# Kernel tuning notes

Measured on AMD Instinct MI355X. Metric: run time of the kernel, lower is better.

Reference implementation:

```python
import math
import jax
import jax.numpy as jnp
import numpy as np

LMAX = 6                 # lmax
F8, F2 = 16, 64          # f_out//8, f_out//2 for f_out=128
DIM6 = sum((2 * l + 1) ** 2 for l in range(LMAX + 1))  # 455 = dim of so3_irreps(6)
NA = NB = NG = 16        # SO(3) activation grid (alpha, beta, gamma)
B, T, H, C = 32, 16, 4, 128


def _real_sh(lmax, xyz):
    # real spherical harmonics: (N,3) unit vectors -> (N,(lmax+1)^2), m=-l..l per l
    x, y, z = xyz[:, 0], xyz[:, 1], xyz[:, 2]
    st = np.sqrt(np.clip(1.0 - z * z, 0.0, None))
    phi = np.arctan2(y, x)
    n = xyz.shape[0]
    P = np.zeros((lmax + 1, lmax + 1, n))
    P[0, 0] = 1.0
    for m in range(1, lmax + 1):
        P[m, m] = -(2 * m - 1) * st * P[m - 1, m - 1]
    for m in range(lmax):
        P[m + 1, m] = (2 * m + 1) * z * P[m, m]
    for m in range(lmax + 1):
        for l in range(m + 2, lmax + 1):
            P[l, m] = ((2 * l - 1) * z * P[l - 1, m] - (l + m - 1) * P[l - 2, m]) / (l - m)
    cols = []
    for l in range(lmax + 1):
        for m in range(-l, l + 1):
            am = abs(m)
            K = math.sqrt((2 * l + 1) / (4 * math.pi) * math.factorial(l - am) / math.factorial(l + am))
            if m > 0:
                cols.append(math.sqrt(2.0) * K * np.cos(m * phi) * P[l, m])
            elif m < 0:
                cols.append(math.sqrt(2.0) * K * np.sin(am * phi) * P[l, am])
            else:
                cols.append(K * P[l, 0])
    return np.stack(cols, axis=-1)


def _flat_wigner(lmax, Rs):
    # component-normalized flat real Wigner-D basis: (G,3,3) -> (G, sum_l (2l+1)^2)
    # D_l(R) solved from Y_l(R x) = D_l(R) Y_l(x) by least squares in float64
    rng = np.random.default_rng(0)
    pts = rng.normal(size=(32, 3))
    pts /= np.linalg.norm(pts, axis=1, keepdims=True)
    Y = _real_sh(lmax, pts)                                     # (32,(lmax+1)^2)
    rp = np.einsum('gij,nj->gni', Rs, pts).reshape(-1, 3)
    Yr = _real_sh(lmax, rp).reshape(len(Rs), 32, -1)            # (G,32,(lmax+1)^2)
    blocks = []
    for l in range(lmax + 1):
        d = 2 * l + 1
        o = l * l
        Apinv = np.linalg.pinv(Y[:, o:o + d])                   # (d,32)
        D = np.einsum('kn,gnm->gmk', Apinv, Yr[:, :, o:o + d])  # (G,d,d)
        blocks.append(math.sqrt(d) * D.reshape(len(Rs), d * d))
    return np.concatenate(blocks, axis=-1)


def _rz(a):
    c, s = np.cos(a), np.sin(a)
    z, o = np.zeros_like(a), np.ones_like(a)
    return np.stack([np.stack([c, -s, z], -1), np.stack([s, c, z], -1), np.stack([z, z, o], -1)], -2)


def _ry(a):
    c, s = np.cos(a), np.sin(a)
    z, o = np.zeros_like(a), np.ones_like(a)
    return np.stack([np.stack([c, z, s], -1), np.stack([z, o, z], -1), np.stack([-s, z, c], -1)], -2)


def _so3_grid():
    # ZYZ Euler grid, Gauss-Legendre in beta; rotations (G,3,3) + Haar weights (G,) summing to 1
    nodes, wts = np.polynomial.legendre.leggauss(NB)
    betas = np.arccos(nodes)
    alphas = np.arange(NA) * 2 * np.pi / NA
    gammas = np.arange(NG) * 2 * np.pi / NG
    Aa, Bb, Cg = np.meshgrid(alphas, betas, gammas, indexing='ij')
    Rs = _rz(Aa.ravel()) @ _ry(Bb.ravel()) @ _rz(Cg.ravel())
    w = np.broadcast_to(wts[None, :, None], (NA, NB, NG)).ravel().copy()
    w *= (2 * np.pi / NA) * (2 * np.pi / NG) / (8 * np.pi ** 2)
    return Rs, w


def _ico_rotations():
    # the 60 rotations of the icosahedral group, generated by closure
    phi = (1.0 + 5.0 ** 0.5) / 2.0
    def rot(axis, ang):
        a = np.asarray(axis, dtype=np.float64)
        a = a / np.linalg.norm(a)
        K = np.array([[0.0, -a[2], a[1]], [a[2], 0.0, -a[0]], [-a[1], a[0], 0.0]])
        return np.eye(3) + math.sin(ang) * K + (1.0 - math.cos(ang)) * (K @ K)
    gens = [rot([0.0, 1.0, phi], 2.0 * np.pi / 5.0), rot([0.0, 0.0, 1.0], np.pi)]
    elems = [np.eye(3)]
    seen = {tuple(np.round(np.eye(3), 5).ravel())}
    frontier = list(elems)
    while frontier:
        nxt = []
        for R in frontier:
            for g in gens:
                Q = g @ R
                k = tuple(np.round(Q, 5).ravel())
                if k not in seen:
                    seen.add(k)
                    elems.append(Q)
                    nxt.append(Q)
        frontier = nxt
    return np.stack(elems)


def _equi_linear(xl, wl):
    # e3nn-style per-irrep linear: xl (...,f_in,u,m), wl (f_in,f_out,u,v); fan_in = f_in*u
    fan_in = wl.shape[0] * wl.shape[2]
    return jnp.einsum('...fum,fguv->...gvm', xl, wl) / np.sqrt(fan_in)


def _forward(x, trajectory, w1s, w1v, w2, D_in, D_outw, ico_wigners):
    b, t, _ = trajectory.shape
    # pack '1x0e+3x1e': scalar = traj[...,9], vectors = traj[...,:9]
    s = trajectory[..., 9][..., None, None, None]       # (b,t,f=1,u=1,m=1)
    v = trajectory[..., :9].reshape(b, t, 1, 3, 3)      # (b,t,f=1,u=3,m=3)
    h = jnp.concatenate([_equi_linear(s, w1s).reshape(b, t, F8, 1),
                         _equi_linear(v, w1v).reshape(b, t, F8, 9)], axis=-1)  # (b,t,16,10)
    # SO(3) activation: coeffs -> grid signal -> relu -> coeffs (lmax 1 -> 6)
    sig = jax.nn.relu(jnp.einsum('btci,gi->btcg', h, D_in))
    h = jnp.einsum('btcg,gi->btci', sig, D_outw)        # (b,t,16,455)
    # per-l equivariant linear, f 16 -> 64
    outs = []
    o = 0
    for l in range(LMAX + 1):
        d = 2 * l + 1
        xl = h[..., o:o + d * d].reshape(b, t, F8, d, d)
        outs.append(_equi_linear(xl, w2[l]).reshape(b, t, F2, d * d))
        o += d * d
    traj = jnp.concatenate(outs, axis=-1)               # (b,t,64,455)
    traj = jnp.einsum('bhcj,ij->bhci', traj, ico_wigners)  # sample on ico rotations
    xg = jnp.einsum('bhcj,ij->bhci', x, ico_wigners)
    return xg, traj


def setup_inputs():
    key = jax.random.key(0)
    ks = jax.random.split(key, 11)
    Rs, w = _so3_grid()
    D_in = _flat_wigner(1, Rs).astype(np.float32)                      # (G,10)
    D_outw = (_flat_wigner(LMAX, Rs) * w[:, None]).astype(np.float32)  # (G,455)
    ico = _flat_wigner(LMAX, _ico_rotations()).astype(np.float32)      # (60,455)
    inp = dict(
        x=jax.random.normal(ks[0], (B, H, C, DIM6), jnp.float32),
        trajectory=jax.random.normal(ks[1], (B, T, 10), jnp.float32),
        w1s=jax.random.normal(ks[2], (1, F8, 1, 1), jnp.float32),
        w1v=jax.random.normal(ks[3], (1, F8, 3, 3), jnp.float32),
        D_in=jnp.asarray(D_in),
        D_outw=jnp.asarray(D_outw),
        ico_wigners=jnp.asarray(ico),
    )
    for l in range(LMAX + 1):
        inp['w2_%d' % l] = jax.random.normal(ks[4 + l], (F8, F2, 2 * l + 1, 2 * l + 1), jnp.float32)
    return inp


def reference(x, trajectory, w1s, w1v, w2_0, w2_1, w2_2, w2_3, w2_4, w2_5, w2_6, D_in, D_outw, ico_wigners):
    w2 = [w2_0, w2_1, w2_2, w2_3, w2_4, w2_5, w2_6]
    return _forward(x, trajectory, w1s, w1v, w2, D_in, D_outw, ico_wigners)
```

## Files before the change

kernel.cpp:

```cpp
#include <hip/hip_runtime.h>
#include <math.h>


#define NBT  512
#define F8c  16
#define F2c  64
#define GJ   455
#define GG   4096
#define NICO 60
#define JP   512

typedef short bf16x8 __attribute__((ext_vector_type(8)));
typedef float f32x4  __attribute__((ext_vector_type(4)));
typedef unsigned int u32;
typedef unsigned short ushort;

struct W7 { const float* p[7]; };

__device__ __forceinline__ ushort f2bf(float f) {
  u32 u = __float_as_uint(f);
  return (ushort)((u + 0x7fffu + ((u >> 16) & 1u)) >> 16);
}

__device__ __forceinline__ int sel7(int l, int a0, int a1, int a2, int a3,
                                    int a4, int a5, int a6) {
  int r = a6;
  r = (l == 5) ? a5 : r; r = (l == 4) ? a4 : r; r = (l == 3) ? a3 : r;
  r = (l == 2) ? a2 : r; r = (l == 1) ? a1 : r; r = (l == 0) ? a0 : r;
  return r;
}

__global__ __launch_bounds__(256) void k_hic(const float* __restrict__ traj,
                                             const float* __restrict__ w1s,
                                             const float* __restrict__ w1v,
                                             const float* __restrict__ ico,
                                             float* __restrict__ h,
                                             ushort* __restrict__ icoB) {
  if (blockIdx.x < 320) {
    int idx = blockIdx.x * 256 + threadIdx.x;
    if (idx >= NBT * 160) return;
    int bt = idx / 160, r = idx % 160, c = r / 10, i = r % 10;
    const float* tr = traj + bt * 10;
    float val;
    if (i == 0) {
      val = tr[9] * w1s[c];
    } else {
      int k = i - 1, v = k / 3, m = k % 3;
      float s = 0.f;
      #pragma unroll
      for (int u = 0; u < 3; ++u) s = fmaf(tr[u * 3 + m], w1v[c * 9 + u * 3 + v], s);
      val = s * 0.57735026918962576f;
    }
    h[idx] = val;
  } else {
    int e = (blockIdx.x - 320) * 256 + threadIdx.x;
    int i = e >> 9, j = e & 511;
    icoB[e] = (i < NICO && j < GJ) ? f2bf(ico[i * GJ + j]) : (ushort)0;
  }
}

__global__ __launch_bounds__(256) void k_bt(const float* __restrict__ Dout,
                                            ushort* __restrict__ DoutBT) {
  __shared__ float t[64][65];
  int jt = blockIdx.x, kt = blockIdx.y;
  int tx = threadIdx.x & 63, ty = threadIdx.x >> 6;
  #pragma unroll
  for (int i = 0; i < 16; ++i) {
    int r = i * 4 + ty, j = jt * 64 + tx;
    t[r][tx] = (j < GJ) ? Dout[(size_t)(kt * 64 + r) * GJ + j] : 0.f;
  }
  __syncthreads();
  #pragma unroll
  for (int i = 0; i < 16; ++i) {
    int jl = i * 4 + ty;
    DoutBT[(size_t)(jt * 64 + jl) * GG + kt * 64 + tx] = f2bf(t[tx][jl]);
  }
}

__global__ __launch_bounds__(256) void k_sig(const float* __restrict__ h,
                                             const float* __restrict__ Din,
                                             ushort* __restrict__ sigb) {
  __shared__ float hs[160];
  int tid = threadIdx.x;
  int mb = blockIdx.y;
  int kt = blockIdx.x;
  if (tid < 160) hs[tid] = h[mb * 160 + tid];
  float dr[80];
  const float4* dp = (const float4*)(Din + (size_t)(kt * 2048 + tid * 8) * 10);
  #pragma unroll
  for (int q = 0; q < 20; ++q) {
    float4 v = dp[q];
    dr[q * 4 + 0] = v.x; dr[q * 4 + 1] = v.y; dr[q * 4 + 2] = v.z; dr[q * 4 + 3] = v.w;
  }
  __syncthreads();
  #pragma unroll
  for (int r = 0; r < 16; ++r) {
    float hv[10];
    #pragma unroll
    for (int i = 0; i < 10; ++i) hv[i] = hs[r * 10 + i];
    bf16x8 o;
    #pragma unroll
    for (int j = 0; j < 8; ++j) {
      float s = 0.f;
      #pragma unroll
      for (int i = 0; i < 10; ++i) s = fmaf(hv[i], dr[j * 10 + i], s);
      o[j] = (short)f2bf(fmaxf(s, 0.f));
    }
    *(bf16x8*)&sigb[((size_t)(mb * 16 + r)) * GG + kt * 2048 + tid * 8] = o;
  }
}

__global__ __launch_bounds__(256) void k_mm2(const ushort* __restrict__ A,
                                             const ushort* __restrict__ Bm,
                                             ushort* __restrict__ Abuf,
                                             int btBase) {
  __shared__ __align__(16) short Asb[2][64 * 64];
  __shared__ __align__(16) short Bsb[2][64 * 64];
  int tid = threadIdx.x;
  int lane = tid & 63, wid = tid >> 6;
  int quad = lane >> 4, lr = lane & 15;
  int wm = wid >> 1, wn = wid & 1;
  int bid = blockIdx.x;
  int mb = bid & 63;
  int nb = bid >> 6;

  f32x4 acc[2][2];
  #pragma unroll
  for (int a = 0; a < 2; ++a)
    #pragma unroll
    for (int b = 0; b < 2; ++b) acc[a][b] = (f32x4){0.f, 0.f, 0.f, 0.f};

  const ushort* Ab = A + (size_t)mb * 64 * GG;
  const ushort* Bb = Bm + (size_t)nb * 64 * GG;

  auto stage = [&](int buf, int kc) {
    #pragma unroll
    for (int it = 0; it < 2; ++it) {
      int s0 = (wid * 2 + it) * 64;
      int s = s0 + lane;
      int r = s >> 3, pp = s & 7, p = pp ^ (r & 7);
      __builtin_amdgcn_global_load_lds(
          (const __attribute__((address_space(1))) u32*)(Ab + (size_t)r * GG + kc + p * 8),
          (__attribute__((address_space(3))) u32*)(&Asb[buf][s0 * 8]), 16, 0, 0);
    }
    #pragma unroll
    for (int it = 0; it < 2; ++it) {
      int s0 = (wid * 2 + it) * 64;
      int s = s0 + lane;
      int r = s >> 3, pp = s & 7, p = pp ^ (r & 7);
      __builtin_amdgcn_global_load_lds(
          (const __attribute__((address_space(1))) u32*)(Bb + (size_t)r * GG + kc + p * 8),
          (__attribute__((address_space(3))) u32*)(&Bsb[buf][s0 * 8]), 16, 0, 0);
    }
  };

  stage(0, 0);
  __syncthreads();
  for (int it = 0; it < 64; ++it) {
    int cur = it & 1;
    if (it < 63) stage(cur ^ 1, (it + 1) * 64);
    #pragma unroll
    for (int ks = 0; ks < 2; ++ks) {
      bf16x8 af[2], bv[2];
      #pragma unroll
      for (int mt = 0; mt < 2; ++mt) {
        int ra = wm * 32 + mt * 16 + lr;
        int v = (ks * 4 + quad) ^ (ra & 7);
        af[mt] = *(const bf16x8*)&Asb[cur][(ra * 8 + v) * 8];
      }
      #pragma unroll
      for (int nt = 0; nt < 2; ++nt) {
        int rb = wn * 32 + nt * 16 + lr;
        int v = (ks * 4 + quad) ^ (rb & 7);
        bv[nt] = *(const bf16x8*)&Bsb[cur][(rb * 8 + v) * 8];
      }
      #pragma unroll
      for (int mt = 0; mt < 2; ++mt)
        #pragma unroll
        for (int nt = 0; nt < 2; ++nt)
          acc[mt][nt] = __builtin_amdgcn_mfma_f32_16x16x32_bf16(af[mt], bv[nt], acc[mt][nt], 0, 0, 0);
    }
    __syncthreads();
  }
  #pragma unroll
  for (int nt = 0; nt < 2; ++nt) {
    int j = nb * 64 + wn * 32 + nt * 16 + lr;
    if (j < GJ) {
      int l = (j >= 1) + (j >= 10) + (j >= 35) + (j >= 84) + (j >= 165) + (j >= 286);
      int o    = sel7(l, 0, 1, 10, 35, 84, 165, 286);
      int d    = sel7(l, 1, 3, 5, 7, 9, 11, 13);
      int Kp   = sel7(l, 64, 64, 128, 128, 192, 192, 256);
      int Aoff = sel7(l, 0, 32768, 131072, 458752, 917504, 1802240, 2883584);
      int jl = j - o;
      float rcpd = 1.0f / (float)d;
      int u = (int)(((float)jl + 0.5f) * rcpd);
      int mB = jl - u * d;
      #pragma unroll
      for (int mt = 0; mt < 2; ++mt)
        #pragma unroll
        for (int r = 0; r < 4; ++r) {
          int m = mb * 64 + wm * 32 + mt * 16 + quad * 4 + r;
          int btg = btBase + (m >> 4), f = m & 15;
          Abuf[(size_t)Aoff + ((size_t)btg * d + mB) * Kp + f * d + u] =
              f2bf(acc[mt][nt][r]);
        }
    }
  }
}


__global__ __launch_bounds__(256) void k_wT(W7 w2, ushort* __restrict__ Bbuf) {
  int ee = blockIdx.x * 256 + threadIdx.x;
  if (ee >= 573440) return;
  int l = (ee >= 4096) + (ee >= 16384) + (ee >= 57344) + (ee >= 114688) +
          (ee >= 225280) + (ee >= 360448);
  int base = sel7(l, 0, 4096, 16384, 57344, 114688, 225280, 360448);
  int d    = sel7(l, 1, 3, 5, 7, 9, 11, 13);
  int Kp   = sel7(l, 64, 64, 128, 128, 192, 192, 256);
  int local = ee - base;
  int row = local / Kp, kcol = local - row * Kp;
  int g2 = row / d, v = row - g2 * d;
  ushort val = 0;
  if (kcol < 16 * d) {
    int f = kcol / d, u = kcol - f * d;
    const float* wl = w2.p[l];
    float scl = rsqrtf(16.f * (float)d);
    val = f2bf(wl[(((size_t)f * 64 + g2) * d + u) * d + v] * scl);
  }
  Bbuf[ee] = val;
}

__global__ __launch_bounds__(256) void k_batch(const ushort* __restrict__ Abuf,
                                               const ushort* __restrict__ Bbuf,
                                               ushort* __restrict__ trajbf) {
  __shared__ __align__(16) short As[64 * 64];
  __shared__ __align__(16) short Bs[64 * 64];
  int bid = blockIdx.x;
  int l = (bid >= 8) + (bid >= 80) + (bid >= 280) + (bid >= 672) +
          (bid >= 1320) + (bid >= 2288);
  int bbase = sel7(l, 0, 8, 80, 280, 672, 1320, 2288);
  int d     = sel7(l, 1, 3, 5, 7, 9, 11, 13);
  int Kp    = sel7(l, 64, 64, 128, 128, 192, 192, 256);
  int o     = sel7(l, 0, 1, 10, 35, 84, 165, 286);
  int Aoff  = sel7(l, 0, 32768, 131072, 458752, 917504, 1802240, 2883584);
  int Boff  = sel7(l, 0, 4096, 16384, 57344, 114688, 225280, 360448);
  int t = bid - bbase;
  int mtile = t / d, ntile = t - mtile * d;

  int tid = threadIdx.x;
  int lane = tid & 63, wid = tid >> 6;
  int quad = lane >> 4, lr = lane & 15;
  int wm = wid >> 1, wn = wid & 1;

  f32x4 acc[2][2];
  #pragma unroll
  for (int a = 0; a < 2; ++a)
    #pragma unroll
    for (int b = 0; b < 2; ++b) acc[a][b] = (f32x4){0.f, 0.f, 0.f, 0.f};

  const ushort* Ab = Abuf + Aoff;
  const ushort* Bb = Bbuf + Boff;

  for (int kc = 0; kc < Kp; kc += 64) {
    __syncthreads();
    #pragma unroll
    for (int it = 0; it < 2; ++it) {
      int s0 = (wid * 2 + it) * 64;
      int s = s0 + lane;
      int r = s >> 3, p8 = s & 7, p = p8 ^ (r & 7);
      const ushort* ga = Ab + (size_t)(mtile * 64 + r) * Kp + kc + p * 8;
      __builtin_amdgcn_global_load_lds(
          (const __attribute__((address_space(1))) u32*)ga,
          (__attribute__((address_space(3))) u32*)(As + s0 * 8), 16, 0, 0);
      const ushort* gb = Bb + (size_t)(ntile * 64 + r) * Kp + kc + p * 8;
      __builtin_amdgcn_global_load_lds(
          (const __attribute__((address_space(1))) u32*)gb,
          (__attribute__((address_space(3))) u32*)(Bs + s0 * 8), 16, 0, 0);
    }
    __syncthreads();
    #pragma unroll
    for (int ks = 0; ks < 2; ++ks) {
      int v = (ks * 4 + quad) ^ (lr & 7);
      bf16x8 af[2], bfv[2];
      #pragma unroll
      for (int mt = 0; mt < 2; ++mt)
        af[mt] = *(const bf16x8*)&As[(wm * 32 + mt * 16 + lr) * 64 + v * 8];
      #pragma unroll
      for (int nt = 0; nt < 2; ++nt)
        bfv[nt] = *(const bf16x8*)&Bs[(wn * 32 + nt * 16 + lr) * 64 + v * 8];
      #pragma unroll
      for (int mt = 0; mt < 2; ++mt)
        #pragma unroll
        for (int nt = 0; nt < 2; ++nt)
          acc[mt][nt] = __builtin_amdgcn_mfma_f32_16x16x32_bf16(af[mt], bfv[nt], acc[mt][nt], 0, 0, 0);
    }
  }
  #pragma unroll
  for (int mt = 0; mt < 2; ++mt)
    #pragma unroll
    for (int nt = 0; nt < 2; ++nt)
      #pragma unroll
      for (int r = 0; r < 4; ++r) {
        int Mrow = mtile * 64 + wm * 32 + mt * 16 + quad * 4 + r;
        int Ncol = ntile * 64 + wn * 32 + nt * 16 + lr;
        int bt = Mrow / d, m = Mrow - bt * d;
        int g2 = Ncol / d, v = Ncol - g2 * d;
        trajbf[(size_t)(bt * 64 + g2) * JP + o + v * d + m] = f2bf(acc[mt][nt][r]);
      }
}

__global__ __launch_bounds__(256) void k_ico(const ushort* __restrict__ trajbf,
                                             const float* __restrict__ x,
                                             const ushort* __restrict__ icoB,
                                             float* __restrict__ trajo,
                                             float* __restrict__ xg) {
  __shared__ __align__(16) short As[64 * 64];
  __shared__ __align__(16) short Bs[64 * 64];
  bool isX = blockIdx.x >= 512;
  int mtile = isX ? (blockIdx.x - 512) : blockIdx.x;
  int tid = threadIdx.x;
  int lane = tid & 63, wid = tid >> 6;
  int quad = lane >> 4, lr = lane & 15;
  int wm = wid >> 1, wn = wid & 1;
  f32x4 acc[2][2];
  #pragma unroll
  for (int a = 0; a < 2; ++a)
    #pragma unroll
    for (int b = 0; b < 2; ++b) acc[a][b] = (f32x4){0.f, 0.f, 0.f, 0.f};
  for (int kc = 0; kc < JP; kc += 64) {
    __syncthreads();
    if (isX) {
      #pragma unroll
      for (int it = 0; it < 2; ++it) {
        int s = it * 256 + tid;
        int r = s >> 3, p8 = s & 7, p = p8 ^ (r & 7);
        const float* xr = x + (size_t)(mtile * 64 + r) * GJ;
        int j0 = kc + p * 8;
        bf16x8 v8;
        #pragma unroll
        for (int jj = 0; jj < 8; ++jj) {
          int j = j0 + jj;
          v8[jj] = (j < GJ) ? (short)f2bf(xr[j]) : (short)0;
        }
        *(bf16x8*)&As[s * 8] = v8;
      }
    } else {
      #pragma unroll
      for (int it = 0; it < 2; ++it) {
        int s0 = (wid * 2 + it) * 64;
        int s = s0 + lane;
        int r = s >> 3, p8 = s & 7, p = p8 ^ (r & 7);
        const ushort* ga = trajbf + (size_t)(mtile * 64 + r) * JP + kc + p * 8;
        __builtin_amdgcn_global_load_lds(
            (const __attribute__((address_space(1))) u32*)ga,
            (__attribute__((address_space(3))) u32*)(As + s0 * 8), 16, 0, 0);
      }
    }
    #pragma unroll
    for (int it = 0; it < 2; ++it) {
      int s0 = (wid * 2 + it) * 64;
      int s = s0 + lane;
      int r = s >> 3, p8 = s & 7, p = p8 ^ (r & 7);
      const ushort* gb = icoB + (size_t)r * JP + kc + p * 8;
      __builtin_amdgcn_global_load_lds(
          (const __attribute__((address_space(1))) u32*)gb,
          (__attribute__((address_space(3))) u32*)(Bs + s0 * 8), 16, 0, 0);
    }
    __syncthreads();
    #pragma unroll
    for (int ks = 0; ks < 2; ++ks) {
      int v = (ks * 4 + quad) ^ (lr & 7);
      bf16x8 af[2], bfv[2];
      #pragma unroll
      for (int mt = 0; mt < 2; ++mt)
        af[mt] = *(const bf16x8*)&As[(wm * 32 + mt * 16 + lr) * 64 + v * 8];
      #pragma unroll
      for (int nt = 0; nt < 2; ++nt)
        bfv[nt] = *(const bf16x8*)&Bs[(wn * 32 + nt * 16 + lr) * 64 + v * 8];
      #pragma unroll
      for (int mt = 0; mt < 2; ++mt)
        #pragma unroll
        for (int nt = 0; nt < 2; ++nt)
          acc[mt][nt] = __builtin_amdgcn_mfma_f32_16x16x32_bf16(af[mt], bfv[nt], acc[mt][nt], 0, 0, 0);
    }
  }
  float* outp = isX ? xg : trajo;
  #pragma unroll
  for (int mt = 0; mt < 2; ++mt)
    #pragma unroll
    for (int nt = 0; nt < 2; ++nt) {
      int i = wn * 32 + nt * 16 + lr;
      if (i < NICO) {
        #pragma unroll
        for (int r = 0; r < 4; ++r) {
          int row = mtile * 64 + wm * 32 + mt * 16 + quad * 4 + r;
          outp[(size_t)row * NICO + i] = acc[mt][nt][r];
        }
      }
    }
}

extern "C" void kernel_launch(void* const* d_in, const int* in_sizes, int n_in,
                              void* d_out, int out_size, void* d_ws, size_t ws_size,
                              hipStream_t stream) {
  const float *x = nullptr, *traj = nullptr, *w1s = nullptr, *w1v = nullptr;
  const float *Din = nullptr, *Dout = nullptr, *ico = nullptr;
  W7 w2{};
  for (int i = 0; i < n_in; ++i) {
    const float* p = (const float*)d_in[i];
    switch (in_sizes[i]) {
      case 7454720: x = p; break;
      case 5120:    traj = p; break;
      case 16:      w1s = p; break;
      case 144:     w1v = p; break;
      case 40960:   Din = p; break;
      case 1863680: Dout = p; break;
      case 27300:   ico = p; break;
      case 1024:    w2.p[0] = p; break;
      case 9216:    w2.p[1] = p; break;
      case 25600:   w2.p[2] = p; break;
      case 50176:   w2.p[3] = p; break;
      case 82944:   w2.p[4] = p; break;
      case 123904:  w2.p[5] = p; break;
      case 173056:  w2.p[6] = p; break;
      default: break;
    }
  }
  char* wsb = (char*)d_ws;
  float*  h       = (float*)wsb;
  ushort* DoutBT  = (ushort*)(wsb + 327680);
  ushort* icoB    = (ushort*)(wsb + 4521984);
  ushort* Abuf    = (ushort*)(wsb + 4587520);
  ushort* Bbuf    = (ushort*)(wsb + 13762560);
  ushort* trajbf  = (ushort*)(wsb + 14909440);
  ushort* sigb    = trajbf;
  float* xg    = (float*)d_out;
  float* trajo = (float*)d_out + 983040;

  hipMemsetAsync(Abuf, 0, 9175040, stream);
  k_hic  <<<dim3(448),    dim3(256), 0, stream>>>(traj, w1s, w1v, ico, h, icoB);
  k_bt   <<<dim3(8, 64),  dim3(256), 0, stream>>>(Dout, DoutBT);
  for (int half = 0; half < 2; ++half) {
    k_sig <<<dim3(2, 256), dim3(256), 0, stream>>>(h + (size_t)half * 40960, Din, sigb);
    k_mm2 <<<dim3(512),    dim3(256), 0, stream>>>(sigb, DoutBT, Abuf, half * 256);
  }
  k_wT   <<<dim3(2240),   dim3(256), 0, stream>>>(w2, Bbuf);
  k_batch<<<dim3(3640),   dim3(256), 0, stream>>>(Abuf, Bbuf, trajbf);
  k_ico  <<<dim3(768),    dim3(256), 0, stream>>>(trajbf, x, icoB, trajo, xg);
}
```

Before: 270.0 us.

## Merge prep kernels, enlarge mm2 tiles to 128x128, and overlap x-projection with batch GEMM

Folds the memset, Dout transpose, w2 reorder, h computation and ico conversion into one prep kernel to cut launch overhead. The sigma-by-Dout GEMM moves from 64x64 to 128x128 tiles with 4x4 MFMA accumulators per wave, and runs as a single pass when the workspace is large enough. The x·ico projection moves into the batched GEMM launch so it runs alongside that work rather than in the final kernel. The larger tiles use more registers and LDS, and the single-pass mm2 has only 256 blocks, which may leave some CUs idle.

Result: faster. 261.9 us (-3.0%).

```diff
diff --git a/kernel.cpp b/kernel.cpp
--- a/kernel.cpp
+++ b/kernel.cpp
@@ -30,50 +30,77 @@
   return r;
 }
 
-__global__ __launch_bounds__(256) void k_hic(const float* __restrict__ traj,
+__global__ __launch_bounds__(256) void k_pre(const float* __restrict__ traj,
                                              const float* __restrict__ w1s,
                                              const float* __restrict__ w1v,
                                              const float* __restrict__ ico,
+                                             const float* __restrict__ Dout,
+                                             W7 w2,
                                              float* __restrict__ h,
-                                             ushort* __restrict__ icoB) {
-  if (blockIdx.x < 320) {
-    int idx = blockIdx.x * 256 + threadIdx.x;
-    if (idx >= NBT * 160) return;
-    int bt = idx / 160, r = idx % 160, c = r / 10, i = r % 10;
-    const float* tr = traj + bt * 10;
-    float val;
-    if (i == 0) {
-      val = tr[9] * w1s[c];
-    } else {
-      int k = i - 1, v = k / 3, m = k % 3;
-      float s = 0.f;
-      #pragma unroll
-      for (int u = 0; u < 3; ++u) s = fmaf(tr[u * 3 + m], w1v[c * 9 + u * 3 + v], s);
-      val = s * 0.57735026918962576f;
-    }
-    h[idx] = val;
+                                             ushort* __restrict__ icoB,
+                                             ushort* __restrict__ DoutBT,
+                                             ushort* __restrict__ Abuf,
+                                             ushort* __restrict__ Bbuf) {
+  __shared__ float t[64][65];
+  int b = blockIdx.x, tid = threadIdx.x;
+  if (b < 2240) {
+    ((uint4*)Abuf)[b * 256 + tid] = (uint4){0, 0, 0, 0};
+  } else if (b < 2752) {
+    int b2 = b - 2240;
+    int jt = b2 & 7, kt = b2 >> 3;
+    int tx = tid & 63, ty = tid >> 6;
+    #pragma unroll
+    for (int i = 0; i < 16; ++i) {
+      int r = i * 4 + ty, j = jt * 64 + tx;
+      t[r][tx] = (j < GJ) ? Dout[(size_t)(kt * 64 + r) * GJ + j] : 0.f;
+    }
+    __syncthreads();
+    #pragma unroll
+    for (int i = 0; i < 16; ++i) {
+      int jl = i * 4 + ty;
+      DoutBT[(size_t)(jt * 64 + jl) * GG + kt * 64 + tx] = f2bf(t[tx][jl]);
+    }
+  } else if (b < 4992) {
+    int ee = (b - 2752) * 256 + tid;
+    if (ee < 573440) {
+      int l = (ee >= 4096) + (ee >= 16384) + (ee >= 57344) + (ee >= 114688) +
+              (ee >= 225280) + (ee >= 360448);
+      int base = sel7(l, 0, 4096, 16384, 57344, 114688, 225280, 360448);
+      int d    = sel7(l, 1, 3, 5, 7, 9, 11, 13);
+      int Kp   = sel7(l, 64, 64, 128, 128, 192, 192, 256);
+      int local = ee - base;
+      int row = local / Kp, kcol = local - row * Kp;
+      int g2 = row / d, v = row - g2 * d;
+      ushort val = 0;
+      if (kcol < 16 * d) {
+        int f = kcol / d, u = kcol - f * d;
+        const float* wl = w2.p[l];
+        float scl = rsqrtf(16.f * (float)d);
+        val = f2bf(wl[(((size_t)f * 64 + g2) * d + u) * d + v] * scl);
+      }
+      Bbuf[ee] = val;
+    }
+  } else if (b < 5312) {
+    int idx = (b - 4992) * 256 + tid;
+    if (idx < NBT * 160) {
+      int bt = idx / 160, r = idx % 160, c = r / 10, i = r % 10;
+      const float* tr = traj + bt * 10;
+      float val;
+      if (i == 0) {
+        val = tr[9] * w1s[c];
+      } else {
+        int k = i - 1, v = k / 3, m = k % 3;
+        float s = 0.f;
+        #pragma unroll
+        for (int u = 0; u < 3; ++u) s = fmaf(tr[u * 3 + m], w1v[c * 9 + u * 3 + v], s);
+        val = s * 0.57735026918962576f;
+      }
+      h[idx] = val;
+    }
   } else {
-    int e = (blockIdx.x - 320) * 256 + threadIdx.x;
+    int e = (b - 5312) * 256 + tid;
     int i = e >> 9, j = e & 511;
     icoB[e] = (i < NICO && j < GJ) ? f2bf(ico[i * GJ + j]) : (ushort)0;
-  }
-}
-
-__global__ __launch_bounds__(256) void k_bt(const float* __restrict__ Dout,
-                                            ushort* __restrict__ DoutBT) {
-  __shared__ float t[64][65];
-  int jt = blockIdx.x, kt = blockIdx.y;
-  int tx = threadIdx.x & 63, ty = threadIdx.x >> 6;
-  #pragma unroll
-  for (int i = 0; i < 16; ++i) {
-    int r = i * 4 + ty, j = jt * 64 + tx;
-    t[r][tx] = (j < GJ) ? Dout[(size_t)(kt * 64 + r) * GJ + j] : 0.f;
-  }
-  __syncthreads();
-  #pragma unroll
-  for (int i = 0; i < 16; ++i) {
-    int jl = i * 4 + ty;
-    DoutBT[(size_t)(jt * 64 + jl) * GG + kt * 64 + tx] = f2bf(t[tx][jl]);
   }
 }
 
@@ -113,30 +140,30 @@
 __global__ __launch_bounds__(256) void k_mm2(const ushort* __restrict__ A,
                                              const ushort* __restrict__ Bm,
                                              ushort* __restrict__ Abuf,
-                                             int btBase) {
-  __shared__ __align__(16) short Asb[2][64 * 64];
-  __shared__ __align__(16) short Bsb[2][64 * 64];
+                                             int btBase, int mbShift) {
+  __shared__ __align__(16) short Asb[2][128 * 64];
+  __shared__ __align__(16) short Bsb[2][128 * 64];
   int tid = threadIdx.x;
   int lane = tid & 63, wid = tid >> 6;
   int quad = lane >> 4, lr = lane & 15;
   int wm = wid >> 1, wn = wid & 1;
   int bid = blockIdx.x;
-  int mb = bid & 63;
-  int nb = bid >> 6;
-
-  f32x4 acc[2][2];
-  #pragma unroll
-  for (int a = 0; a < 2; ++a)
-    #pragma unroll
-    for (int b = 0; b < 2; ++b) acc[a][b] = (f32x4){0.f, 0.f, 0.f, 0.f};
-
-  const ushort* Ab = A + (size_t)mb * 64 * GG;
-  const ushort* Bb = Bm + (size_t)nb * 64 * GG;
+  int mb = bid & ((1 << mbShift) - 1);
+  int nb = bid >> mbShift;
+
+  f32x4 acc[4][4];
+  #pragma unroll
+  for (int a = 0; a < 4; ++a)
+    #pragma unroll
+    for (int b = 0; b < 4; ++b) acc[a][b] = (f32x4){0.f, 0.f, 0.f, 0.f};
+
+  const ushort* Ab = A + (size_t)mb * 128 * GG;
+  const ushort* Bb = Bm + (size_t)nb * 128 * GG;
 
   auto stage = [&](int buf, int kc) {
     #pragma unroll
-    for (int it = 0; it < 2; ++it) {
-      int s0 = (wid * 2 + it) * 64;
+    for (int it = 0; it < 4; ++it) {
+      int s0 = (wid * 4 + it) * 64;
       int s = s0 + lane;
       int r = s >> 3, pp = s & 7, p = pp ^ (r & 7);
       __builtin_amdgcn_global_load_lds(
@@ -144,8 +171,8 @@
           (__attribute__((address_space(3))) u32*)(&Asb[buf][s0 * 8]), 16, 0, 0);
     }
     #pragma unroll
-    for (int it = 0; it < 2; ++it) {
-      int s0 = (wid * 2 + it) * 64;
+    for (int it = 0; it < 4; ++it) {
+      int s0 = (wid * 4 + it) * 64;
       int s = s0 + lane;
       int r = s >> 3, pp = s & 7, p = pp ^ (r & 7);
       __builtin_amdgcn_global_load_lds(
@@ -161,30 +188,30 @@
     if (it < 63) stage(cur ^ 1, (it + 1) * 64);
     #pragma unroll
     for (int ks = 0; ks < 2; ++ks) {
-      bf16x8 af[2], bv[2];
-      #pragma unroll
-      for (int mt = 0; mt < 2; ++mt) {
-        int ra = wm * 32 + mt * 16 + lr;
+      bf16x8 af[4], bv[4];
+      #pragma unroll
+      for (int mt = 0; mt < 4; ++mt) {
+        int ra = wm * 64 + mt * 16 + lr;
         int v = (ks * 4 + quad) ^ (ra & 7);
         af[mt] = *(const bf16x8*)&Asb[cur][(ra * 8 + v) * 8];
       }
       #pragma unroll
-      for (int nt = 0; nt < 2; ++nt) {
-        int rb = wn * 32 + nt * 16 + lr;
+      for (int nt = 0; nt < 4; ++nt) {
+        int rb = wn * 64 + nt * 16 + lr;
         int v = (ks * 4 + quad) ^ (rb & 7);
         bv[nt] = *(const bf16x8*)&Bsb[cur][(rb * 8 + v) * 8];
       }
       #pragma unroll
-      for (int mt = 0; mt < 2; ++mt)
-        #pragma unroll
-        for (int nt = 0; nt < 2; ++nt)
+      for (int mt = 0; mt < 4; ++mt)
+        #pragma unroll
+        for (int nt = 0; nt < 4; ++nt)
           acc[mt][nt] = __builtin_amdgcn_mfma_f32_16x16x32_bf16(af[mt], bv[nt], acc[mt][nt], 0, 0, 0);
     }
     __syncthreads();
   }
   #pragma unroll
-  for (int nt = 0; nt < 2; ++nt) {
-    int j = nb * 64 + wn * 32 + nt * 16 + lr;
+  for (int nt = 0; nt < 4; ++nt) {
+    int j = nb * 128 + wn * 64 + nt * 16 + lr;
     if (j < GJ) {
       int l = (j >= 1) + (j >= 10) + (j >= 35) + (j >= 84) + (j >= 165) + (j >= 286);
       int o    = sel7(l, 0, 1, 10, 35, 84, 165, 286);
@@ -196,10 +223,10 @@
       int u = (int)(((float)jl + 0.5f) * rcpd);
       int mB = jl - u * d;
       #pragma unroll
-      for (int mt = 0; mt < 2; ++mt)
+      for (int mt = 0; mt < 4; ++mt)
         #pragma unroll
         for (int r = 0; r < 4; ++r) {
-          int m = mb * 64 + wm * 32 + mt * 16 + quad * 4 + r;
+          int m = mb * 128 + wm * 64 + mt * 16 + quad * 4 + r;
           int btg = btBase + (m >> 4), f = m & 15;
           Abuf[(size_t)Aoff + ((size_t)btg * d + mB) * Kp + f * d + u] =
               f2bf(acc[mt][nt][r]);
@@ -208,34 +235,87 @@
   }
 }
 
-
-__global__ __launch_bounds__(256) void k_wT(W7 w2, ushort* __restrict__ Bbuf) {
-  int ee = blockIdx.x * 256 + threadIdx.x;
-  if (ee >= 573440) return;
-  int l = (ee >= 4096) + (ee >= 16384) + (ee >= 57344) + (ee >= 114688) +
-          (ee >= 225280) + (ee >= 360448);
-  int base = sel7(l, 0, 4096, 16384, 57344, 114688, 225280, 360448);
-  int d    = sel7(l, 1, 3, 5, 7, 9, 11, 13);
-  int Kp   = sel7(l, 64, 64, 128, 128, 192, 192, 256);
-  int local = ee - base;
-  int row = local / Kp, kcol = local - row * Kp;
-  int g2 = row / d, v = row - g2 * d;
-  ushort val = 0;
-  if (kcol < 16 * d) {
-    int f = kcol / d, u = kcol - f * d;
-    const float* wl = w2.p[l];
-    float scl = rsqrtf(16.f * (float)d);
-    val = f2bf(wl[(((size_t)f * 64 + g2) * d + u) * d + v] * scl);
-  }
-  Bbuf[ee] = val;
-}
-
-__global__ __launch_bounds__(256) void k_batch(const ushort* __restrict__ Abuf,
-                                               const ushort* __restrict__ Bbuf,
-                                               ushort* __restrict__ trajbf) {
+__global__ __launch_bounds__(256) void k_batchX(const ushort* __restrict__ Abuf,
+                                                const ushort* __restrict__ Bbuf,
+                                                const float* __restrict__ x,
+                                                const ushort* __restrict__ icoB,
+                                                ushort* __restrict__ trajbf,
+                                                float* __restrict__ xg) {
   __shared__ __align__(16) short As[64 * 64];
   __shared__ __align__(16) short Bs[64 * 64];
   int bid = blockIdx.x;
+  int tid = threadIdx.x;
+  int lane = tid & 63, wid = tid >> 6;
+  int quad = lane >> 4, lr = lane & 15;
+  int wm = wid >> 1, wn = wid & 1;
+  f32x4 acc[2][2];
+  #pragma unroll
+  for (int a = 0; a < 2; ++a)
+    #pragma unroll
+    for (int b = 0; b < 2; ++b) acc[a][b] = (f32x4){0.f, 0.f, 0.f, 0.f};
+
+  if (bid >= 3640) {
+    int mtile = bid - 3640;
+    for (int kc = 0; kc < JP; kc += 64) {
+      __syncthreads();
+      #pragma unroll
+      for (int it = 0; it < 2; ++it) {
+        int s = it * 256 + tid;
+        int r = s >> 3, p8 = s & 7, p = p8 ^ (r & 7);
+        const float* xr = x + (size_t)(mtile * 64 + r) * GJ;
+        int j0 = kc + p * 8;
+        bf16x8 v8;
+        #pragma unroll
+        for (int jj = 0; jj < 8; ++jj) {
+          int j = j0 + jj;
+          v8[jj] = (j < GJ) ? (short)f2bf(xr[j]) : (short)0;
+        }
+        *(bf16x8*)&As[s * 8] = v8;
+      }
+      #pragma unroll
+      for (int it = 0; it < 2; ++it) {
+        int s0 = (wid * 2 + it) * 64;
+        int s = s0 + lane;
+        int r = s >> 3, p8 = s & 7, p = p8 ^ (r & 7);
+        const ushort* gb = icoB + (size_t)r * JP + kc + p * 8;
+        __builtin_amdgcn_global_load_lds(
+            (const __attribute__((address_space(1))) u32*)gb,
+            (__attribute__((address_space(3))) u32*)(Bs + s0 * 8), 16, 0, 0);
+      }
+      __syncthreads();
+      #pragma unroll
+      for (int ks = 0; ks < 2; ++ks) {
+        int v = (ks * 4 + quad) ^ (lr & 7);
+        bf16x8 af[2], bfv[2];
+        #pragma unroll
+        for (int mt = 0; mt < 2; ++mt)
+          af[mt] = *(const bf16x8*)&As[(wm * 32 + mt * 16 + lr) * 64 + v * 8];
+        #pragma unroll
+        for (int nt = 0; nt < 2; ++nt)
+          bfv[nt] = *(const bf16x8*)&Bs[(wn * 32 + nt * 16 + lr) * 64 + v * 8];
+        #pragma unroll
+        for (int mt = 0; mt < 2; ++mt)
+          #pragma unroll
+          for (int nt = 0; nt < 2; ++nt)
+            acc[mt][nt] = __builtin_amdgcn_mfma_f32_16x16x32_bf16(af[mt], bfv[nt], acc[mt][nt], 0, 0, 0);
+      }
+    }
+    #pragma unroll
+    for (int mt = 0; mt < 2; ++mt)
+      #pragma unroll
+      for (int nt = 0; nt < 2; ++nt) {
+        int i = wn * 32 + nt * 16 + lr;
+        if (i < NICO) {
+          #pragma unroll
+          for (int r = 0; r < 4; ++r) {
+            int row = mtile * 64 + wm * 32 + mt * 16 + quad * 4 + r;
+            xg[(size_t)row * NICO + i] = acc[mt][nt][r];
+          }
+        }
+      }
+    return;
+  }
+
   int l = (bid >= 8) + (bid >= 80) + (bid >= 280) + (bid >= 672) +
           (bid >= 1320) + (bid >= 2288);
   int bbase = sel7(l, 0, 8, 80, 280, 672, 1320, 2288);
@@ -247,17 +327,6 @@
   int t = bid - bbase;
   int mtile = t / d, ntile = t - mtile * d;
 
-  int tid = threadIdx.x;
-  int lane = tid & 63, wid = tid >> 6;
-  int quad = lane >> 4, lr = lane & 15;
-  int wm = wid >> 1, wn = wid & 1;
-
-  f32x4 acc[2][2];
-  #pragma unroll
-  for (int a = 0; a < 2; ++a)
-    #pragma unroll
-    for (int b = 0; b < 2; ++b) acc[a][b] = (f32x4){0.f, 0.f, 0.f, 0.f};
-
   const ushort* Ab = Abuf + Aoff;
   const ushort* Bb = Bbuf + Boff;
 
@@ -309,15 +378,12 @@
       }
 }
 
-__global__ __launch_bounds__(256) void k_ico(const ushort* __restrict__ trajbf,
-                                             const float* __restrict__ x,
-                                             const ushort* __restrict__ icoB,
-                                             float* __restrict__ trajo,
-                                             float* __restrict__ xg) {
+__global__ __launch_bounds__(256) void k_icoT(const ushort* __restrict__ trajbf,
+                                              const ushort* __restrict__ icoB,
+                                              float* __restrict__ trajo) {
   __shared__ __align__(16) short As[64 * 64];
   __shared__ __align__(16) short Bs[64 * 64];
-  bool isX = blockIdx.x >= 512;
-  int mtile = isX ? (blockIdx.x - 512) : blockIdx.x;
+  int mtile = blockIdx.x;
   int tid = threadIdx.x;
   int lane = tid & 63, wid = tid >> 6;
   int quad = lane >> 4, lr = lane & 15;
@@ -329,38 +395,15 @@
     for (int b = 0; b < 2; ++b) acc[a][b] = (f32x4){0.f, 0.f, 0.f, 0.f};
   for (int kc = 0; kc < JP; kc += 64) {
     __syncthreads();
-    if (isX) {
-      #pragma unroll
-      for (int it = 0; it < 2; ++it) {
-        int s = it * 256 + tid;
-        int r = s >> 3, p8 = s & 7, p = p8 ^ (r & 7);
-        const float* xr = x + (size_t)(mtile * 64 + r) * GJ;
-        int j0 = kc + p * 8;
-        bf16x8 v8;
-        #pragma unroll
-        for (int jj = 0; jj < 8; ++jj) {
-          int j = j0 + jj;
-          v8[jj] = (j < GJ) ? (short)f2bf(xr[j]) : (short)0;
-        }
-        *(bf16x8*)&As[s * 8] = v8;
-      }
-    } else {
-      #pragma unroll
-      for (int it = 0; it < 2; ++it) {
-        int s0 = (wid * 2 + it) * 64;
-        int s = s0 + lane;
-        int r = s >> 3, p8 = s & 7, p = p8 ^ (r & 7);
-        const ushort* ga = trajbf + (size_t)(mtile * 64 + r) * JP + kc + p * 8;
-        __builtin_amdgcn_global_load_lds(
-            (const __attribute__((address_space(1))) u32*)ga,
-            (__attribute__((address_space(3))) u32*)(As + s0 * 8), 16, 0, 0);
-      }
-    }
     #pragma unroll
     for (int it = 0; it < 2; ++it) {
       int s0 = (wid * 2 + it) * 64;
       int s = s0 + lane;
       int r = s >> 3, p8 = s & 7, p = p8 ^ (r & 7);
+      const ushort* ga = trajbf + (size_t)(mtile * 64 + r) * JP + kc + p * 8;
+      __builtin_amdgcn_global_load_lds(
+          (const __attribute__((address_space(1))) u32*)ga,
+          (__attribute__((address_space(3))) u32*)(As + s0 * 8), 16, 0, 0);
       const ushort* gb = icoB + (size_t)r * JP + kc + p * 8;
       __builtin_amdgcn_global_load_lds(
           (const __attribute__((address_space(1))) u32*)gb,
@@ -384,7 +427,6 @@
           acc[mt][nt] = __builtin_amdgcn_mfma_f32_16x16x32_bf16(af[mt], bfv[nt], acc[mt][nt], 0, 0, 0);
     }
   }
-  float* outp = isX ? xg : trajo;
   #pragma unroll
   for (int mt = 0; mt < 2; ++mt)
     #pragma unroll
@@ -394,7 +436,7 @@
         #pragma unroll
         for (int r = 0; r < 4; ++r) {
           int row = mtile * 64 + wm * 32 + mt * 16 + quad * 4 + r;
-          outp[(size_t)row * NICO + i] = acc[mt][nt][r];
+          trajo[(size_t)row * NICO + i] = acc[mt][nt][r];
         }
       }
     }
@@ -432,19 +474,22 @@
   ushort* icoB    = (ushort*)(wsb + 4521984);
   ushort* Abuf    = (ushort*)(wsb + 4587520);
   ushort* Bbuf    = (ushort*)(wsb + 13762560);
-  ushort* trajbf  = (ushort*)(wsb + 14909440);
-  ushort* sigb    = trajbf;
+  ushort* sigb    = (ushort*)(wsb + 14909440);
+  ushort* trajbf  = sigb;
   float* xg    = (float*)d_out;
   float* trajo = (float*)d_out + 983040;
 
-  hipMemsetAsync(Abuf, 0, 9175040, stream);
-  k_hic  <<<dim3(448),    dim3(256), 0, stream>>>(traj, w1s, w1v, ico, h, icoB);
-  k_bt   <<<dim3(8, 64),  dim3(256), 0, stream>>>(Dout, DoutBT);
-  for (int half = 0; half < 2; ++half) {
-    k_sig <<<dim3(2, 256), dim3(256), 0, stream>>>(h + (size_t)half * 40960, Din, sigb);
-    k_mm2 <<<dim3(512),    dim3(256), 0, stream>>>(sigb, DoutBT, Abuf, half * 256);
-  }
-  k_wT   <<<dim3(2240),   dim3(256), 0, stream>>>(w2, Bbuf);
-  k_batch<<<dim3(3640),   dim3(256), 0, stream>>>(Abuf, Bbuf, trajbf);
-  k_ico  <<<dim3(768),    dim3(256), 0, stream>>>(trajbf, x, icoB, trajo, xg);
-}
+  k_pre<<<dim3(5440), dim3(256), 0, stream>>>(traj, w1s, w1v, ico, Dout, w2,
+                                              h, icoB, DoutBT, Abuf, Bbuf);
+  if (ws_size >= 82018304ULL) {
+    k_sig<<<dim3(2, 512), dim3(256), 0, stream>>>(h, Din, sigb);
+    k_mm2<<<dim3(256),    dim3(256), 0, stream>>>(sigb, DoutBT, Abuf, 0, 6);
+  } else {
+    for (int half = 0; half < 2; ++half) {
+      k_sig<<<dim3(2, 256), dim3(256), 0, stream>>>(h + (size_t)half * 40960, Din, sigb);
+      k_mm2<<<dim3(128),    dim3(256), 0, stream>>>(sigb, DoutBT, Abuf, half * 256, 5);
+    }
+  }
+  k_batchX<<<dim3(3896), dim3(256), 0, stream>>>(Abuf, Bbuf, x, icoB, trajbf, xg);
+  k_icoT  <<<dim3(512),  dim3(256), 0, stream>>>(trajbf, icoB, trajo);
+}
```
